# Kernel optimization log

Measured on AMD Instinct MI355X. Metric: run time of the kernel, lower is better.

The kernel has to match this reference:

```python
import jax, jax.numpy as jnp
import numpy as np

WINDOW = 16
NUM_HEADS = 4
DIM = 256
LN_EPS = 1e-5


def setup_inputs() -> dict:
    key = jax.random.key(0)
    ks = jax.random.split(key, 8)
    B, C, N = 8, DIM, 16384
    s = 1.0 / np.sqrt(C)
    x = jax.random.normal(ks[0], (B, C, N), dtype=jnp.float32)
    in_proj_w = jax.random.uniform(ks[1], (3 * C, C), minval=-s, maxval=s, dtype=jnp.float32)
    in_proj_b = jnp.zeros((3 * C,), dtype=jnp.float32)
    out_proj_w = jax.random.uniform(ks[2], (C, C), minval=-s, maxval=s, dtype=jnp.float32)
    out_proj_b = jnp.zeros((C,), dtype=jnp.float32)
    ln_g = jnp.ones((C,), dtype=jnp.float32)
    ln_b = jnp.zeros((C,), dtype=jnp.float32)
    return {"x": x, "in_proj_w": in_proj_w, "in_proj_b": in_proj_b,
            "out_proj_w": out_proj_w, "out_proj_b": out_proj_b,
            "ln_g": ln_g, "ln_b": ln_b}


def _swin_attn_1d(x, in_proj_w, in_proj_b, out_proj_w, out_proj_b, ln_g, ln_b):
    B, C, N = x.shape
    W = WINDOW
    H = NUM_HEADS
    hd = C // H
    xt = jnp.transpose(x, (0, 2, 1))                      # [B, N, C]
    pad_len = (W - N % W) % W                             # static Python int
    if pad_len > 0:
        xt = jnp.pad(xt, ((0, 0), (0, pad_len), (0, 0)))
    N_pad = N + pad_len
    nw = B * (N_pad // W)
    xw = xt.reshape(nw, W, C)                             # [nw, W, C]
    # QKV projection (torch MHA: x @ in_proj_w.T + in_proj_b)
    qkv = jnp.einsum('nwc,dc->nwd', xw, in_proj_w) + in_proj_b  # [nw, W, 3C]
    q, k, v = jnp.split(qkv, 3, axis=-1)
    q = q.reshape(nw, W, H, hd) * (1.0 / np.sqrt(hd))
    k = k.reshape(nw, W, H, hd)
    v = v.reshape(nw, W, H, hd)
    scores = jnp.einsum('nqhd,nkhd->nhqk', q, k)          # [nw, H, W, W]
    probs = jax.nn.softmax(scores, axis=-1)
    attn = jnp.einsum('nhqk,nkhd->nqhd', probs, v).reshape(nw, W, C)
    attn = jnp.einsum('nwc,dc->nwd', attn, out_proj_w) + out_proj_b
    # residual + LayerNorm
    y = attn + xw
    mu = jnp.mean(y, axis=-1, keepdims=True)
    var = jnp.mean(jnp.square(y - mu), axis=-1, keepdims=True)
    y = (y - mu) * jax.lax.rsqrt(var + LN_EPS) * ln_g + ln_b
    y = y.reshape(B, N_pad, C)
    if pad_len > 0:
        y = y[:, :N, :]
    return jnp.transpose(y, (0, 2, 1))                    # [B, C, N]


def reference(x, in_proj_w, in_proj_b, out_proj_w, out_proj_b, ln_g, ln_b):
    return _swin_attn_1d(x, in_proj_w, in_proj_b, out_proj_w, out_proj_b, ln_g, ln_b)
```

## Files before the change

kernel.cpp:

```cpp
#include <hip/hip_runtime.h>


#define C_DIM 256
#define NSEQ  16384

typedef __attribute__((ext_vector_type(8))) short bf16x8;
typedef __attribute__((ext_vector_type(4))) float f32x4;

__device__ __forceinline__ unsigned short f2bf(float f) {
    unsigned int u = __builtin_bit_cast(unsigned int, f);
    u += 0x7FFFu + ((u >> 16) & 1u);
    return (unsigned short)(u >> 16);
}
__device__ __forceinline__ float bf2f(unsigned short h) {
    unsigned int u = ((unsigned int)h) << 16;
    return __builtin_bit_cast(float, u);
}
__device__ __forceinline__ unsigned int pack2(float a, float b) {
    return ((unsigned int)f2bf(b) << 16) | (unsigned int)f2bf(a);
}
__device__ __forceinline__ int xsw(int row, int col) {
    return col ^ (((row >> 3) & 1) << 4);
}

__global__ void prep_weights(const float* __restrict__ wq_f, const float* __restrict__ wo_f,
                             unsigned short* __restrict__ wq, unsigned short* __restrict__ wo) {
    int i = blockIdx.x * 256 + threadIdx.x;
    if (i < 768 * 256) {
        int nt = i >> 12, r = i & 4095;
        int k = r >> 9, r2 = r & 511;
        int l = r2 >> 5, r3 = r2 & 31;
        wq[i] = f2bf(wq_f[(nt * 16 + l) * 256 + k * 32 + r3]);
    }
    if (i < 256 * 256) {
        int nt = i >> 12, r = i & 4095;
        int k = r >> 9, r2 = r & 511;
        int l = r2 >> 5, r3 = r2 & 31;
        wo[i] = f2bf(wo_f[(nt * 16 + l) * 256 + k * 32 + r3]);
    }
}

__global__ __launch_bounds__(512, 4) void swin_fused(
    const float* __restrict__ x,
    const unsigned short* __restrict__ wq,
    const unsigned short* __restrict__ wo,
    const float* __restrict__ bq,
    const float* __restrict__ bo,
    const float* __restrict__ lng,
    const float* __restrict__ lnb,
    float* __restrict__ out)
{
    __shared__ __align__(16) unsigned short lds_x[32][264];
    __shared__ __align__(16) unsigned short lds_qk[32][520];
    __shared__ __align__(16) unsigned short lds_vt[256][40];
    __shared__ __align__(16) unsigned short lds_p[8][16][16];
    __shared__ float lds_mean[32];
    __shared__ float lds_rstd[32];

    const int tid  = threadIdx.x;
    const int wv   = tid >> 6;
    const int lane = tid & 63;
    const int l15  = lane & 15;
    const int quad = lane >> 4;

    const int w0    = blockIdx.x * 2;
    const int batch = w0 >> 10;
    const int nbase = (w0 & 1023) << 4;
    const long xbase = (long)batch * ((long)C_DIM * NSEQ) + nbase;

    {
        const int t4 = (tid & 7) << 2;
        const int c4 = (tid >> 3) << 2;
        float4 r[4];
        #pragma unroll
        for (int j = 0; j < 4; ++j)
            r[j] = *reinterpret_cast<const float4*>(&x[xbase + (long)(c4 + j) * NSEQ + t4]);
        const float* rf = reinterpret_cast<const float*>(r);
        #pragma unroll
        for (int i = 0; i < 4; ++i) {
            uint2 v;
            v.x = pack2(rf[0 * 4 + i], rf[1 * 4 + i]);
            v.y = pack2(rf[2 * 4 + i], rf[3 * 4 + i]);
            *reinterpret_cast<uint2*>(&lds_x[t4 + i][xsw(t4 + i, c4)]) = v;
        }
    }

    const unsigned short* wqbase = wq + l15 * 32 + quad * 8;
    bf16x8 bfr[8];
    #pragma unroll
    for (int k = 0; k < 8; ++k)
        bfr[k] = *reinterpret_cast<const bf16x8*>(wqbase + wv * 4096 + k * 512);

    __syncthreads();

    bf16x8 xa0[8], xa1[8];
    #pragma unroll
    for (int k = 0; k < 8; ++k) {
        xa0[k] = *reinterpret_cast<const bf16x8*>(&lds_x[l15][xsw(l15, k * 32 + quad * 8)]);
        xa1[k] = *reinterpret_cast<const bf16x8*>(&lds_x[16 + l15][xsw(16 + l15, k * 32 + quad * 8)]);
    }

    for (int i = 0; i < 6; ++i) {
        const int nt = (i << 3) + wv;
        const int d  = nt * 16 + l15;
        if (i) {
            #pragma unroll
            for (int k = 0; k < 8; ++k)
                bfr[k] = *reinterpret_cast<const bf16x8*>(wqbase + nt * 4096 + k * 512);
        }
        const float bias = bq[d];
        f32x4 acc0 = {bias, bias, bias, bias};
        f32x4 acc1 = {bias, bias, bias, bias};
        #pragma unroll
        for (int k = 0; k < 8; ++k) {
            acc0 = __builtin_amdgcn_mfma_f32_16x16x32_bf16(xa0[k], bfr[k], acc0, 0, 0, 0);
            acc1 = __builtin_amdgcn_mfma_f32_16x16x32_bf16(xa1[k], bfr[k], acc1, 0, 0, 0);
        }
        if (d < 512) {
            #pragma unroll
            for (int r = 0; r < 4; ++r) {
                const int r0 = quad * 4 + r;
                lds_qk[r0][xsw(r0, d)]           = f2bf(acc0[r]);
                lds_qk[16 + r0][xsw(16 + r0, d)] = f2bf(acc1[r]);
            }
        } else {
            #pragma unroll
            for (int r = 0; r < 4; ++r) {
                lds_vt[d - 512][quad * 4 + r]      = f2bf(acc0[r]);
                lds_vt[d - 512][16 + quad * 4 + r] = f2bf(acc1[r]);
            }
        }
    }
    __syncthreads();

    {
        const int g = wv >> 2;
        const int h = wv & 3;
        f32x4 sc = {0.f, 0.f, 0.f, 0.f};
        #pragma unroll
        for (int kk = 0; kk < 2; ++kk) {
            const int row = g * 16 + l15;
            bf16x8 aq = *reinterpret_cast<const bf16x8*>(&lds_qk[row][xsw(row, h * 64 + kk * 32 + quad * 8)]);
            bf16x8 bk = *reinterpret_cast<const bf16x8*>(&lds_qk[row][xsw(row, 256 + h * 64 + kk * 32 + quad * 8)]);
            sc = __builtin_amdgcn_mfma_f32_16x16x32_bf16(aq, bk, sc, 0, 0, 0);
        }
        #pragma unroll
        for (int r = 0; r < 4; ++r) {
            float s = sc[r] * 0.125f;
            float m = s;
            #pragma unroll
            for (int msk = 1; msk <= 8; msk <<= 1) m = fmaxf(m, __shfl_xor(m, msk, 16));
            float e = __expf(s - m);
            float su = e;
            #pragma unroll
            for (int msk = 1; msk <= 8; msk <<= 1) su += __shfl_xor(su, msk, 16);
            lds_p[wv][quad * 4 + r][l15] = f2bf(e / su);
        }
        bf16x8 ap = {0,0,0,0,0,0,0,0};
        if (quad < 2) ap = *reinterpret_cast<const bf16x8*>(&lds_p[wv][l15][quad * 8]);
        #pragma unroll
        for (int dt = 0; dt < 4; ++dt) {
            bf16x8 bv = {0,0,0,0,0,0,0,0};
            if (quad < 2)
                bv = *reinterpret_cast<const bf16x8*>(&lds_vt[h * 64 + dt * 16 + l15][g * 16 + quad * 8]);
            f32x4 acc = {0.f, 0.f, 0.f, 0.f};
            acc = __builtin_amdgcn_mfma_f32_16x16x32_bf16(ap, bv, acc, 0, 0, 0);
            #pragma unroll
            for (int r = 0; r < 4; ++r) {
                const int row = g * 16 + quad * 4 + r;
                lds_qk[row][xsw(row, h * 64 + dt * 16 + l15)] = f2bf(acc[r]);
            }
        }
    }

    const unsigned short* wobase = wo + l15 * 32 + quad * 8;
    bf16x8 wfr[8];
    #pragma unroll
    for (int k = 0; k < 8; ++k)
        wfr[k] = *reinterpret_cast<const bf16x8*>(wobase + wv * 4096 + k * 512);

    __syncthreads();

    unsigned short* ldy = &lds_vt[0][0];
    bf16x8 aa0[8], aa1[8];
    #pragma unroll
    for (int k = 0; k < 8; ++k) {
        aa0[k] = *reinterpret_cast<const bf16x8*>(&lds_qk[l15][xsw(l15, k * 32 + quad * 8)]);
        aa1[k] = *reinterpret_cast<const bf16x8*>(&lds_qk[16 + l15][xsw(16 + l15, k * 32 + quad * 8)]);
    }
    for (int i = 0; i < 2; ++i) {
        const int nt = (i << 3) + wv;
        const int d  = nt * 16 + l15;
        if (i) {
            #pragma unroll
            for (int k = 0; k < 8; ++k)
                wfr[k] = *reinterpret_cast<const bf16x8*>(wobase + nt * 4096 + k * 512);
        }
        const float bias = bo[d];
        f32x4 acc0 = {bias, bias, bias, bias};
        f32x4 acc1 = {bias, bias, bias, bias};
        #pragma unroll
        for (int k = 0; k < 8; ++k) {
            acc0 = __builtin_amdgcn_mfma_f32_16x16x32_bf16(aa0[k], wfr[k], acc0, 0, 0, 0);
            acc1 = __builtin_amdgcn_mfma_f32_16x16x32_bf16(aa1[k], wfr[k], acc1, 0, 0, 0);
        }
        #pragma unroll
        for (int r = 0; r < 4; ++r) {
            const int r0 = quad * 4 + r;
            ldy[r0 * 264 + xsw(r0, d)] =
                f2bf(acc0[r] + bf2f(lds_x[r0][xsw(r0, d)]));
            ldy[(16 + r0) * 264 + xsw(16 + r0, d)] =
                f2bf(acc1[r] + bf2f(lds_x[16 + r0][xsw(16 + r0, d)]));
        }
    }
    __syncthreads();

    {
        const int row = tid >> 4, part = tid & 15;
        float s = 0.f, sq = 0.f;
        #pragma unroll
        for (int half = 0; half < 2; ++half) {
            bf16x8 yv = *reinterpret_cast<const bf16x8*>(&ldy[row * 264 + xsw(row, part * 16 + half * 8)]);
            #pragma unroll
            for (int ii = 0; ii < 8; ++ii) {
                float v = bf2f((unsigned short)yv[ii]);
                s += v; sq += v * v;
            }
        }
        #pragma unroll
        for (int msk = 1; msk <= 8; msk <<= 1) {
            s  += __shfl_xor(s,  msk, 16);
            sq += __shfl_xor(sq, msk, 16);
        }
        if (part == 0) {
            float mean = s * (1.0f / 256.0f);
            float var  = sq * (1.0f / 256.0f) - mean * mean;
            lds_mean[row] = mean;
            lds_rstd[row] = rsqrtf(var + 1e-5f);
        }
    }
    __syncthreads();

    {
        const int t4 = (tid & 7) << 2;
        const int c0 = tid >> 3;
        float mean[4], rstd[4];
        #pragma unroll
        for (int i = 0; i < 4; ++i) { mean[i] = lds_mean[t4 + i]; rstd[i] = lds_rstd[t4 + i]; }
        #pragma unroll
        for (int it = 0; it < 4; ++it) {
            const int c = c0 + (it << 6);
            const float g = lng[c], b = lnb[c];
            float4 o;
            float* of = reinterpret_cast<float*>(&o);
            #pragma unroll
            for (int i = 0; i < 4; ++i)
                of[i] = (bf2f(ldy[(t4 + i) * 264 + xsw(t4 + i, c)]) - mean[i]) * rstd[i] * g + b;
            *reinterpret_cast<float4*>(&out[xbase + (long)c * NSEQ + t4]) = o;
        }
    }
}

extern "C" void kernel_launch(void* const* d_in, const int* in_sizes, int n_in,
                              void* d_out, int out_size, void* d_ws, size_t ws_size,
                              hipStream_t stream) {
    const float* x   = (const float*)d_in[0];
    const float* ipw = (const float*)d_in[1];
    const float* ipb = (const float*)d_in[2];
    const float* opw = (const float*)d_in[3];
    const float* opb = (const float*)d_in[4];
    const float* lng = (const float*)d_in[5];
    const float* lnb = (const float*)d_in[6];
    float* out = (float*)d_out;

    unsigned short* wq = (unsigned short*)d_ws;
    unsigned short* wo = wq + 768 * 256;

    prep_weights<<<768, 256, 0, stream>>>(ipw, opw, wq, wo);
    swin_fused<<<4096, 512, 0, stream>>>(x, wq, wo, ipb, opb, lng, lnb, out);
}
```

Baseline: 368.2 us.

## Process four windows per block with 16 waves and vectorized LDS stores

The fused kernel now handles 64 tokens (four windows) per 1024-thread block. Each wave owns one 16-column output tile of Q, K, V and the output projection, and streams activation fragments from LDS across four row tiles. This reuses each weight fragment load across twice as many rows. The MFMA operands are swapped so accumulators hold four consecutive columns, which lets results be packed into 8-byte LDS stores instead of scalar 2-byte stores. In exchange the block needs more LDS, which may reduce occupancy.

```diff
diff --git a/kernel.cpp b/kernel.cpp
--- a/kernel.cpp
+++ b/kernel.cpp
@@ -18,6 +18,9 @@
 }
 __device__ __forceinline__ unsigned int pack2(float a, float b) {
     return ((unsigned int)f2bf(b) << 16) | (unsigned int)f2bf(a);
+}
+__device__ __forceinline__ uint2 pack4(f32x4 v) {
+    uint2 r; r.x = pack2(v[0], v[1]); r.y = pack2(v[2], v[3]); return r;
 }
 __device__ __forceinline__ int xsw(int row, int col) {
     return col ^ (((row >> 3) & 1) << 4);
@@ -40,7 +43,7 @@
     }
 }
 
-__global__ __launch_bounds__(512, 4) void swin_fused(
+__global__ __launch_bounds__(1024, 4) void swin_fused(
     const float* __restrict__ x,
     const unsigned short* __restrict__ wq,
     const unsigned short* __restrict__ wo,
@@ -50,12 +53,12 @@
     const float* __restrict__ lnb,
     float* __restrict__ out)
 {
-    __shared__ __align__(16) unsigned short lds_x[32][264];
-    __shared__ __align__(16) unsigned short lds_qk[32][520];
-    __shared__ __align__(16) unsigned short lds_vt[256][40];
-    __shared__ __align__(16) unsigned short lds_p[8][16][16];
-    __shared__ float lds_mean[32];
-    __shared__ float lds_rstd[32];
+    __shared__ __align__(16) unsigned short lds_x[64][264];
+    __shared__ __align__(16) unsigned short lds_qk[64][520];
+    __shared__ __align__(16) unsigned short lds_vt[256][72];
+    __shared__ __align__(16) unsigned short lds_p[16][16][16];
+    __shared__ float lds_mean[64];
+    __shared__ float lds_rstd[64];
 
     const int tid  = threadIdx.x;
     const int wv   = tid >> 6;
@@ -63,14 +66,14 @@
     const int l15  = lane & 15;
     const int quad = lane >> 4;
 
-    const int w0    = blockIdx.x * 2;
+    const int w0    = blockIdx.x * 4;
     const int batch = w0 >> 10;
     const int nbase = (w0 & 1023) << 4;
     const long xbase = (long)batch * ((long)C_DIM * NSEQ) + nbase;
 
     {
-        const int t4 = (tid & 7) << 2;
-        const int c4 = (tid >> 3) << 2;
+        const int t4 = (tid & 15) << 2;
+        const int c4 = (tid >> 4) << 2;
         float4 r[4];
         #pragma unroll
         for (int j = 0; j < 4; ++j)
@@ -86,60 +89,88 @@
     }
 
     const unsigned short* wqbase = wq + l15 * 32 + quad * 8;
-    bf16x8 bfr[8];
+    bf16x8 wA[8], wB[8];
     #pragma unroll
     for (int k = 0; k < 8; ++k)
-        bfr[k] = *reinterpret_cast<const bf16x8*>(wqbase + wv * 4096 + k * 512);
-
-    __syncthreads();
-
-    bf16x8 xa0[8], xa1[8];
-    #pragma unroll
-    for (int k = 0; k < 8; ++k) {
-        xa0[k] = *reinterpret_cast<const bf16x8*>(&lds_x[l15][xsw(l15, k * 32 + quad * 8)]);
-        xa1[k] = *reinterpret_cast<const bf16x8*>(&lds_x[16 + l15][xsw(16 + l15, k * 32 + quad * 8)]);
-    }
-
-    for (int i = 0; i < 6; ++i) {
-        const int nt = (i << 3) + wv;
-        const int d  = nt * 16 + l15;
-        if (i) {
-            #pragma unroll
-            for (int k = 0; k < 8; ++k)
-                bfr[k] = *reinterpret_cast<const bf16x8*>(wqbase + nt * 4096 + k * 512);
-        }
-        const float bias = bq[d];
-        f32x4 acc0 = {bias, bias, bias, bias};
-        f32x4 acc1 = {bias, bias, bias, bias};
+        wA[k] = *reinterpret_cast<const bf16x8*>(wqbase + wv * 4096 + k * 512);
+
+    __syncthreads();
+
+    {
+        #pragma unroll
+        for (int k = 0; k < 8; ++k)
+            wB[k] = *reinterpret_cast<const bf16x8*>(wqbase + (16 + wv) * 4096 + k * 512);
+        const float4 b4 = *reinterpret_cast<const float4*>(&bq[wv * 16 + quad * 4]);
+        f32x4 acc[4];
+        #pragma unroll
+        for (int s = 0; s < 4; ++s) acc[s] = {b4.x, b4.y, b4.z, b4.w};
         #pragma unroll
         for (int k = 0; k < 8; ++k) {
-            acc0 = __builtin_amdgcn_mfma_f32_16x16x32_bf16(xa0[k], bfr[k], acc0, 0, 0, 0);
-            acc1 = __builtin_amdgcn_mfma_f32_16x16x32_bf16(xa1[k], bfr[k], acc1, 0, 0, 0);
-        }
-        if (d < 512) {
-            #pragma unroll
-            for (int r = 0; r < 4; ++r) {
-                const int r0 = quad * 4 + r;
-                lds_qk[r0][xsw(r0, d)]           = f2bf(acc0[r]);
-                lds_qk[16 + r0][xsw(16 + r0, d)] = f2bf(acc1[r]);
-            }
-        } else {
-            #pragma unroll
-            for (int r = 0; r < 4; ++r) {
-                lds_vt[d - 512][quad * 4 + r]      = f2bf(acc0[r]);
-                lds_vt[d - 512][16 + quad * 4 + r] = f2bf(acc1[r]);
-            }
-        }
+            #pragma unroll
+            for (int s = 0; s < 4; ++s) {
+                const int row = s * 16 + l15;
+                bf16x8 a = *reinterpret_cast<const bf16x8*>(&lds_x[row][xsw(row, k * 32 + quad * 8)]);
+                acc[s] = __builtin_amdgcn_mfma_f32_16x16x32_bf16(wA[k], a, acc[s], 0, 0, 0);
+            }
+        }
+        const int cb = wv * 16 + quad * 4;
+        #pragma unroll
+        for (int s = 0; s < 4; ++s) {
+            const int row = s * 16 + l15;
+            *reinterpret_cast<uint2*>(&lds_qk[row][xsw(row, cb)]) = pack4(acc[s]);
+        }
+    }
+    {
+        #pragma unroll
+        for (int k = 0; k < 8; ++k)
+            wA[k] = *reinterpret_cast<const bf16x8*>(wqbase + (32 + wv) * 4096 + k * 512);
+        const float4 b4 = *reinterpret_cast<const float4*>(&bq[256 + wv * 16 + quad * 4]);
+        f32x4 acc[4];
+        #pragma unroll
+        for (int s = 0; s < 4; ++s) acc[s] = {b4.x, b4.y, b4.z, b4.w};
+        #pragma unroll
+        for (int k = 0; k < 8; ++k) {
+            #pragma unroll
+            for (int s = 0; s < 4; ++s) {
+                const int row = s * 16 + l15;
+                bf16x8 a = *reinterpret_cast<const bf16x8*>(&lds_x[row][xsw(row, k * 32 + quad * 8)]);
+                acc[s] = __builtin_amdgcn_mfma_f32_16x16x32_bf16(wB[k], a, acc[s], 0, 0, 0);
+            }
+        }
+        const int cb = 256 + wv * 16 + quad * 4;
+        #pragma unroll
+        for (int s = 0; s < 4; ++s) {
+            const int row = s * 16 + l15;
+            *reinterpret_cast<uint2*>(&lds_qk[row][xsw(row, cb)]) = pack4(acc[s]);
+        }
+    }
+    {
+        const float bias = bq[512 + wv * 16 + l15];
+        f32x4 acc[4];
+        #pragma unroll
+        for (int s = 0; s < 4; ++s) acc[s] = {bias, bias, bias, bias};
+        #pragma unroll
+        for (int k = 0; k < 8; ++k) {
+            #pragma unroll
+            for (int s = 0; s < 4; ++s) {
+                const int row = s * 16 + l15;
+                bf16x8 a = *reinterpret_cast<const bf16x8*>(&lds_x[row][xsw(row, k * 32 + quad * 8)]);
+                acc[s] = __builtin_amdgcn_mfma_f32_16x16x32_bf16(a, wA[k], acc[s], 0, 0, 0);
+            }
+        }
+        #pragma unroll
+        for (int s = 0; s < 4; ++s)
+            *reinterpret_cast<uint2*>(&lds_vt[wv * 16 + l15][s * 16 + quad * 4]) = pack4(acc[s]);
     }
     __syncthreads();
 
     {
         const int g = wv >> 2;
         const int h = wv & 3;
+        const int row = g * 16 + l15;
         f32x4 sc = {0.f, 0.f, 0.f, 0.f};
         #pragma unroll
         for (int kk = 0; kk < 2; ++kk) {
-            const int row = g * 16 + l15;
             bf16x8 aq = *reinterpret_cast<const bf16x8*>(&lds_qk[row][xsw(row, h * 64 + kk * 32 + quad * 8)]);
             bf16x8 bk = *reinterpret_cast<const bf16x8*>(&lds_qk[row][xsw(row, 256 + h * 64 + kk * 32 + quad * 8)]);
             sc = __builtin_amdgcn_mfma_f32_16x16x32_bf16(aq, bk, sc, 0, 0, 0);
@@ -164,53 +195,45 @@
             if (quad < 2)
                 bv = *reinterpret_cast<const bf16x8*>(&lds_vt[h * 64 + dt * 16 + l15][g * 16 + quad * 8]);
             f32x4 acc = {0.f, 0.f, 0.f, 0.f};
-            acc = __builtin_amdgcn_mfma_f32_16x16x32_bf16(ap, bv, acc, 0, 0, 0);
-            #pragma unroll
-            for (int r = 0; r < 4; ++r) {
-                const int row = g * 16 + quad * 4 + r;
-                lds_qk[row][xsw(row, h * 64 + dt * 16 + l15)] = f2bf(acc[r]);
-            }
+            acc = __builtin_amdgcn_mfma_f32_16x16x32_bf16(bv, ap, acc, 0, 0, 0);
+            const int cb = h * 64 + dt * 16 + quad * 4;
+            *reinterpret_cast<uint2*>(&lds_qk[row][xsw(row, cb)]) = pack4(acc);
         }
     }
 
     const unsigned short* wobase = wo + l15 * 32 + quad * 8;
-    bf16x8 wfr[8];
     #pragma unroll
     for (int k = 0; k < 8; ++k)
-        wfr[k] = *reinterpret_cast<const bf16x8*>(wobase + wv * 4096 + k * 512);
+        wA[k] = *reinterpret_cast<const bf16x8*>(wobase + wv * 4096 + k * 512);
 
     __syncthreads();
 
     unsigned short* ldy = &lds_vt[0][0];
-    bf16x8 aa0[8], aa1[8];
-    #pragma unroll
-    for (int k = 0; k < 8; ++k) {
-        aa0[k] = *reinterpret_cast<const bf16x8*>(&lds_qk[l15][xsw(l15, k * 32 + quad * 8)]);
-        aa1[k] = *reinterpret_cast<const bf16x8*>(&lds_qk[16 + l15][xsw(16 + l15, k * 32 + quad * 8)]);
-    }
-    for (int i = 0; i < 2; ++i) {
-        const int nt = (i << 3) + wv;
-        const int d  = nt * 16 + l15;
-        if (i) {
-            #pragma unroll
-            for (int k = 0; k < 8; ++k)
-                wfr[k] = *reinterpret_cast<const bf16x8*>(wobase + nt * 4096 + k * 512);
-        }
-        const float bias = bo[d];
-        f32x4 acc0 = {bias, bias, bias, bias};
-        f32x4 acc1 = {bias, bias, bias, bias};
+    {
+        const float4 b4 = *reinterpret_cast<const float4*>(&bo[wv * 16 + quad * 4]);
+        f32x4 acc[4];
+        #pragma unroll
+        for (int s = 0; s < 4; ++s) acc[s] = {b4.x, b4.y, b4.z, b4.w};
         #pragma unroll
         for (int k = 0; k < 8; ++k) {
-            acc0 = __builtin_amdgcn_mfma_f32_16x16x32_bf16(aa0[k], wfr[k], acc0, 0, 0, 0);
-            acc1 = __builtin_amdgcn_mfma_f32_16x16x32_bf16(aa1[k], wfr[k], acc1, 0, 0, 0);
-        }
-        #pragma unroll
-        for (int r = 0; r < 4; ++r) {
-            const int r0 = quad * 4 + r;
-            ldy[r0 * 264 + xsw(r0, d)] =
-                f2bf(acc0[r] + bf2f(lds_x[r0][xsw(r0, d)]));
-            ldy[(16 + r0) * 264 + xsw(16 + r0, d)] =
-                f2bf(acc1[r] + bf2f(lds_x[16 + r0][xsw(16 + r0, d)]));
+            #pragma unroll
+            for (int s = 0; s < 4; ++s) {
+                const int row = s * 16 + l15;
+                bf16x8 a = *reinterpret_cast<const bf16x8*>(&lds_qk[row][xsw(row, k * 32 + quad * 8)]);
+                acc[s] = __builtin_amdgcn_mfma_f32_16x16x32_bf16(wA[k], a, acc[s], 0, 0, 0);
+            }
+        }
+        const int cb = wv * 16 + quad * 4;
+        #pragma unroll
+        for (int s = 0; s < 4; ++s) {
+            const int row = s * 16 + l15;
+            uint2 xr = *reinterpret_cast<const uint2*>(&lds_x[row][xsw(row, cb)]);
+            f32x4 y;
+            y[0] = acc[s][0] + bf2f((unsigned short)(xr.x & 0xffff));
+            y[1] = acc[s][1] + bf2f((unsigned short)(xr.x >> 16));
+            y[2] = acc[s][2] + bf2f((unsigned short)(xr.y & 0xffff));
+            y[3] = acc[s][3] + bf2f((unsigned short)(xr.y >> 16));
+            *reinterpret_cast<uint2*>(&ldy[row * 264 + xsw(row, cb)]) = pack4(y);
         }
     }
     __syncthreads();
@@ -242,8 +265,8 @@
     __syncthreads();
 
     {
-        const int t4 = (tid & 7) << 2;
-        const int c0 = tid >> 3;
+        const int t4 = (tid & 15) << 2;
+        const int c0 = tid >> 4;
         float mean[4], rstd[4];
         #pragma unroll
         for (int i = 0; i < 4; ++i) { mean[i] = lds_mean[t4 + i]; rstd[i] = lds_rstd[t4 + i]; }
@@ -277,5 +300,5 @@
     unsigned short* wo = wq + 768 * 256;
 
     prep_weights<<<768, 256, 0, stream>>>(ipw, opw, wq, wo);
-    swin_fused<<<4096, 512, 0, stream>>>(x, wq, wo, ipb, opb, lng, lnb, out);
-}
+    swin_fused<<<2048, 1024, 0, stream>>>(x, wq, wo, ipb, opb, lng, lnb, out);
+}
```

New measurement: 352.4 us. 1.04x faster.
